# Performance work log

Measured on AMD Instinct MI355X. Metric: run time of the kernel, lower is better.

The kernel has to match this reference:

```python
import jax, jax.numpy as jnp
import numpy as np

KS = 3  # kernel_size


def _im2col(x):
    # x: (N, C, H, W) -> (N, H*W, C*KS*KS), matching torch unfold (channel-major,
    # kernel-position-minor) ordering with padding=1.
    N, C, H, W = x.shape
    xp = jnp.pad(x, ((0, 0), (0, 0), (1, 1), (1, 1)))
    patches = jnp.stack(
        [xp[:, :, i:i + H, j:j + W] for i in range(KS) for j in range(KS)],
        axis=2,
    )  # (N, C, 9, H, W)
    return patches.reshape(N, C * KS * KS, H * W).transpose(0, 2, 1)


def setup_inputs() -> dict:
    key = jax.random.key(0)
    k1, k2, k3, k4, k5 = jax.random.split(key, 5)
    N, C, H, W = 4, 64, 192, 192
    outC = 3
    return {
        "lr_features": jax.random.normal(k1, (N, C, H, W), dtype=jnp.float32),
        "W1": jax.random.normal(k2, (3, 256), dtype=jnp.float32) * 0.05,
        "b1": jax.random.normal(k3, (256,), dtype=jnp.float32) * 0.05,
        "W2": jax.random.normal(k4, (256, KS * KS * C * outC), dtype=jnp.float32) * 0.05,
        "b2": jax.random.normal(k5, (KS * KS * C * outC,), dtype=jnp.float32) * 0.05,
        "sr_scale": 4,
    }


def reference(lr_features, W1, b1, W2, b2, sr_scale):
    # Integer sr_scale: mask_mat is all-true and pos_mat_small is the s*s grid
    # of sub-pixel offsets [1/s, i/s, j/s] for i, j in [0, s).
    N, C, H, W = lr_features.shape
    s = int(np.ceil(sr_scale))
    inv = 1.0 / float(sr_scale)
    off = jnp.arange(s, dtype=jnp.float32) * inv
    pos = jnp.stack(jnp.meshgrid(off, off, indexing="ij"), axis=-1).reshape(s * s, 2)
    pos = jnp.concatenate(
        [jnp.full((s * s, 1), inv, dtype=jnp.float32), pos], axis=1
    )  # (s^2, 3)

    # Pos2Weight MLP -> per-subpixel dynamic conv weights (s^2, C*9, outC)
    hidden = jax.nn.relu(pos @ W1 + b1)
    local_weight = (hidden @ W2 + b2).reshape(s * s, KS * KS * C, -1)
    outC = local_weight.shape[-1]

    cols = _im2col(lr_features)  # (N, H*W, C*9)
    # batched small matmul: each sub-pixel position has its own filter
    out = jnp.einsum("npk,sko->nspo", cols, local_weight)  # (N, s^2, H*W, outC)
    out = out.reshape(N, s, s, H, W, outC)
    out = out.transpose(0, 5, 3, 1, 4, 2).reshape(N, outC, s * H, s * W)
    return out
```

## Files before the change

### kernel.cpp

```cpp
#include <hip/hip_runtime.h>


#define HH   192
#define WWD  192
#define SS   4
#define OC   3
#define PO   48
#define HID  256
#define W2LD 1728
#define BUFS 21120

typedef short  bf16x8 __attribute__((ext_vector_type(8)));
typedef float  f32x4  __attribute__((ext_vector_type(4)));

static __device__ __forceinline__ short f2bf(float f) {
    unsigned u = __float_as_uint(f);
    unsigned r = (u + 0x7fffu + ((u >> 16) & 1u)) >> 16;
    return (short)r;
}

static __device__ __forceinline__ void pin(bf16x8& v) {
    asm volatile("" : "+v"(v));
}

__global__ __launch_bounds__(256) void prep_kernel(
        const float* __restrict__ x,
        const float* __restrict__ W1, const float* __restrict__ b1,
        const float* __restrict__ W2, const float* __restrict__ b2,
        short* __restrict__ lwb, short* __restrict__ xt) {
    const int b = blockIdx.x;
    const int t = threadIdx.x;
    if (b < 112) {
        __shared__ float hlds[HID];
        const int p = b / 7;
        {
            const float pi = (float)(p >> 2) * 0.25f;
            const float pj = (float)(p & 3) * 0.25f;
            const float v = 0.25f * W1[t] + pi * W1[HID + t] + pj * W1[2 * HID + t]
                          + b1[t];
            hlds[t] = v > 0.f ? v : 0.f;
        }
        __syncthreads();
        const int col = (b % 7) * 256 + t;
        if (col < W2LD) {
            float a = 0.f;
#pragma unroll 32
            for (int hh = 0; hh < HID; ++hh)
                a += hlds[hh] * W2[hh * W2LD + col];
            const int o = col % 3, kc = col / 3;
            const int tap = kc % 9, c = kc / 9;
            lwb[(tap * PO + p * 3 + o) * 64 + c] = f2bf(a + b2[col]);
        }
    } else {
        __shared__ short tl[64][72];
        const int bb = b - 112;
        const int wt = bb % 3;
        const int h  = (bb / 3) % HH;
        const int n  = bb / (3 * HH);
        const int w0 = wt * 64;
#pragma unroll
        for (int i = 0; i < 4; ++i) {
            const int idx = i * 256 + t;
            const int c   = idx >> 4;
            const int j4  = idx & 15;
            const float4 v = *(const float4*)
                &x[(((size_t)(n * 64 + c)) * HH + h) * WWD + w0 + j4 * 4];
            tl[j4 * 4 + 0][c] = f2bf(v.x);
            tl[j4 * 4 + 1][c] = f2bf(v.y);
            tl[j4 * 4 + 2][c] = f2bf(v.z);
            tl[j4 * 4 + 3][c] = f2bf(v.w);
        }
        __syncthreads();
        const int w  = t >> 2;
        const int c0 = (t & 3) * 16;
        short* dst = &xt[(((size_t)n * HH + h) * WWD + w0 + w) * 64 + c0];
        *(bf16x8*)&dst[0] = *(const bf16x8*)&tl[w][c0];
        *(bf16x8*)&dst[8] = *(const bf16x8*)&tl[w][c0 + 8];
    }
}

__global__ __launch_bounds__(384) void meta_up_mfma(
        const short* __restrict__ xt, const short* __restrict__ lwb,
        float* __restrict__ out) {
    __shared__ __align__(16) short smem[2 * BUFS + 18720];
    float* obuf = (float*)&smem[2 * BUFS];

    const int xcd = blockIdx.x & 7;
    const int ii  = blockIdx.x >> 3;
    const int tid = threadIdx.x;
    const int lane = tid & 63;
    const int wv   = (tid >> 6) % 3;
    const int wgq  = (tid >> 6) / 3;
    const int quad = lane >> 4, l15 = lane & 15;

    bf16x8 Bf[18];
#pragma unroll
    for (int tap = 0; tap < 9; ++tap)
#pragma unroll
        for (int kc2 = 0; kc2 < 2; ++kc2)
            Bf[tap * 2 + kc2] = *(const bf16x8*)
                &lwb[(tap * PO + wv * 16 + l15) * 64 + kc2 * 32 + quad * 8];
#pragma unroll
    for (int i = 0; i < 18; ++i) pin(Bf[i]);

    int n_c, h0_c, w0_c;
    {
        const int tau = 96 * xcd + 3 * ii;
        n_c = tau / 192;
        const int rem = tau % 192;
        w0_c = (rem / 64) * 64;
        h0_c = (rem % 64) * 3;
    }

    const bf16x8 z = {0, 0, 0, 0, 0, 0, 0, 0};
    bf16x8 sv[7];

#pragma unroll
    for (int k = 0; k < 7; ++k) {
        const int item = k * 384 + tid;
        const int r  = item / 528;
        const int rm = item - r * 528;
        const int j  = rm >> 3, cb = rm & 7;
        const int gr = h0_c - 1 + r, gc = w0_c - 1 + j;
        const bool ok = (item < 2640) && ((unsigned)gr < (unsigned)HH) &&
                        ((unsigned)gc < (unsigned)WWD);
        sv[k] = ok ? *(const bf16x8*)
            &xt[((size_t)(n_c * HH + gr) * WWD + gc) * 64 + cb * 8] : z;
    }
#pragma unroll
    for (int k = 0; k < 7; ++k) {
        const int item = k * 384 + tid;
        if (item < 2640) {
            const int r  = item / 528;
            const int rm = item - r * 528;
            const int j  = rm >> 3, cb = rm & 7;
            *(bf16x8*)&smem[(r * 66 + j) * 64 + ((cb ^ (j & 7)) << 3)] = sv[k];
        }
    }
    __syncthreads();

    for (int t = 0; t < 3; ++t) {
        int n_n = n_c, h0_n = h0_c, w0_n = w0_c;
        if (t < 2) {
            const int tau = 96 * xcd + 3 * ii + t + 1;
            n_n = tau / 192;
            const int rem = tau % 192;
            w0_n = (rem / 64) * 64;
            h0_n = (rem % 64) * 3;
#pragma unroll
            for (int k = 0; k < 7; ++k) {
                const int item = k * 384 + tid;
                const int r  = item / 528;
                const int rm = item - r * 528;
                const int j  = rm >> 3, cb = rm & 7;
                const int gr = h0_n - 1 + r, gc = w0_n - 1 + j;
                const bool ok = (item < 2640) && ((unsigned)gr < (unsigned)HH) &&
                                ((unsigned)gc < (unsigned)WWD);
                sv[k] = ok ? *(const bf16x8*)
                    &xt[((size_t)(n_n * HH + gr) * WWD + gc) * 64 + cb * 8] : z;
            }
        }

        const short* __restrict__ xb = &smem[(t & 1) * BUFS];
        f32x4 acc[3][2];
#pragma unroll
        for (int ih = 0; ih < 3; ++ih)
#pragma unroll
            for (int mtl = 0; mtl < 2; ++mtl)
                acc[ih][mtl] = (f32x4){0.f, 0.f, 0.f, 0.f};

#pragma unroll
        for (int b = 0; b < 6; ++b) {
            const int dj = b >> 1, kc2 = b & 1;
#pragma unroll
            for (int mtl = 0; mtl < 2; ++mtl) {
                const int mt  = wgq * 2 + mtl;
                const int col = mt * 16 + l15 + dj;
                const int blk = (kc2 * 4 + quad) ^ (col & 7);
#pragma unroll
                for (int r = 0; r < 5; ++r) {
                    bf16x8 a = *(const bf16x8*)&xb[(r * 66 + col) * 64 + (blk << 3)];
#pragma unroll
                    for (int di = 0; di < 3; ++di) {
                        const int ih = r - di;
                        if (ih >= 0 && ih < 3)
                            acc[ih][mtl] = __builtin_amdgcn_mfma_f32_16x16x32_bf16(
                                a, Bf[(di * 3 + dj) * 2 + kc2], acc[ih][mtl], 0, 0, 0);
                    }
                }
            }
        }

        {
            const int po = wv * 16 + l15;
            const int o  = po % 3;
            const int p  = po / 3;
            const int si = p >> 2, sj = p & 3;
            const int osi = o * 4 + si;
#pragma unroll
            for (int ih = 0; ih < 3; ++ih)
#pragma unroll
                for (int mtl = 0; mtl < 2; ++mtl) {
                    const int mt = wgq * 2 + mtl;
#pragma unroll
                    for (int r4 = 0; r4 < 4; ++r4) {
                        const int wl = mt * 16 + quad * 4 + r4;
                        obuf[(ih * 12 + osi) * 260 + wl * 4 + sj] = acc[ih][mtl][r4];
                    }
                }
        }
        __syncthreads();

#pragma unroll
        for (int ih = 0; ih < 3; ++ih)
#pragma unroll
            for (int h2 = 0; h2 < 2; ++h2) {
                const int idx = h2 * 384 + tid;
                const int osi = idx >> 6;
                const int c4  = idx & 63;
                const int o = osi >> 2, si = osi & 3;
                const int hh = h0_c + ih;
                const size_t base =
                    ((size_t)(n_c * OC + o) * (SS * HH) + (size_t)(SS * hh + si))
                        * (SS * WWD) + (size_t)(4 * w0_c) + c4 * 4;
                *(float4*)&out[base] =
                    *(const float4*)&obuf[(ih * 12 + osi) * 260 + c4 * 4];
            }

        if (t < 2) {
#pragma unroll
            for (int k = 0; k < 7; ++k) {
                const int item = k * 384 + tid;
                if (item < 2640) {
                    const int r  = item / 528;
                    const int rm = item - r * 528;
                    const int j  = rm >> 3, cb = rm & 7;
                    *(bf16x8*)&smem[((t + 1) & 1) * BUFS +
                        (r * 66 + j) * 64 + ((cb ^ (j & 7)) << 3)] = sv[k];
                }
            }
            __syncthreads();
            n_c = n_n; h0_c = h0_n; w0_c = w0_n;
        }
    }
}

extern "C" void kernel_launch(void* const* d_in, const int* in_sizes, int n_in,
                              void* d_out, int out_size, void* d_ws, size_t ws_size,
                              hipStream_t stream) {
    const float* x  = (const float*)d_in[0];
    const float* W1 = (const float*)d_in[1];
    const float* b1 = (const float*)d_in[2];
    const float* W2 = (const float*)d_in[3];
    const float* b2 = (const float*)d_in[4];
    float* out = (float*)d_out;
    short* lwb = (short*)d_ws;
    short* xt  = (short*)d_ws + 32768;

    prep_kernel<<<112 + 4 * HH * 3, 256, 0, stream>>>(x, W1, b1, W2, b2, lwb, xt);
    meta_up_mfma<<<256, 384, 0, stream>>>(xt, lwb, out);
}
```

Measured before the change: 112.4 us.

## Fuse NCHW-to-NHWC bf16 transpose into main MFMA kernel's tile loads

Result: slower. 116.0 us (+3.1%).

```diff
diff --git a/kernel.cpp b/kernel.cpp
--- a/kernel.cpp
+++ b/kernel.cpp
@@ -9,6 +9,7 @@
 #define HID  256
 #define W2LD 1728
 #define BUFS 21120
+#define CST  (HH * WWD)
 
 typedef short  bf16x8 __attribute__((ext_vector_type(8)));
 typedef float  f32x4  __attribute__((ext_vector_type(4)));
@@ -23,64 +24,80 @@
     asm volatile("" : "+v"(v));
 }
 
-__global__ __launch_bounds__(256) void prep_kernel(
-        const float* __restrict__ x,
+__global__ __launch_bounds__(256) void lw_kernel(
         const float* __restrict__ W1, const float* __restrict__ b1,
         const float* __restrict__ W2, const float* __restrict__ b2,
-        short* __restrict__ lwb, short* __restrict__ xt) {
+        short* __restrict__ lwb) {
+    __shared__ float hlds[HID];
     const int b = blockIdx.x;
     const int t = threadIdx.x;
-    if (b < 112) {
-        __shared__ float hlds[HID];
-        const int p = b / 7;
-        {
-            const float pi = (float)(p >> 2) * 0.25f;
-            const float pj = (float)(p & 3) * 0.25f;
-            const float v = 0.25f * W1[t] + pi * W1[HID + t] + pj * W1[2 * HID + t]
-                          + b1[t];
-            hlds[t] = v > 0.f ? v : 0.f;
-        }
-        __syncthreads();
-        const int col = (b % 7) * 256 + t;
-        if (col < W2LD) {
-            float a = 0.f;
+    const int p = b / 7;
+    {
+        const float pi = (float)(p >> 2) * 0.25f;
+        const float pj = (float)(p & 3) * 0.25f;
+        const float v = 0.25f * W1[t] + pi * W1[HID + t] + pj * W1[2 * HID + t]
+                      + b1[t];
+        hlds[t] = v > 0.f ? v : 0.f;
+    }
+    __syncthreads();
+    const int col = (b % 7) * 256 + t;
+    if (col < W2LD) {
+        float a = 0.f;
 #pragma unroll 32
-            for (int hh = 0; hh < HID; ++hh)
-                a += hlds[hh] * W2[hh * W2LD + col];
-            const int o = col % 3, kc = col / 3;
-            const int tap = kc % 9, c = kc / 9;
-            lwb[(tap * PO + p * 3 + o) * 64 + c] = f2bf(a + b2[col]);
-        }
-    } else {
-        __shared__ short tl[64][72];
-        const int bb = b - 112;
-        const int wt = bb % 3;
-        const int h  = (bb / 3) % HH;
-        const int n  = bb / (3 * HH);
-        const int w0 = wt * 64;
-#pragma unroll
-        for (int i = 0; i < 4; ++i) {
-            const int idx = i * 256 + t;
-            const int c   = idx >> 4;
-            const int j4  = idx & 15;
-            const float4 v = *(const float4*)
-                &x[(((size_t)(n * 64 + c)) * HH + h) * WWD + w0 + j4 * 4];
-            tl[j4 * 4 + 0][c] = f2bf(v.x);
-            tl[j4 * 4 + 1][c] = f2bf(v.y);
-            tl[j4 * 4 + 2][c] = f2bf(v.z);
-            tl[j4 * 4 + 3][c] = f2bf(v.w);
-        }
-        __syncthreads();
-        const int w  = t >> 2;
-        const int c0 = (t & 3) * 16;
-        short* dst = &xt[(((size_t)n * HH + h) * WWD + w0 + w) * 64 + c0];
-        *(bf16x8*)&dst[0] = *(const bf16x8*)&tl[w][c0];
-        *(bf16x8*)&dst[8] = *(const bf16x8*)&tl[w][c0 + 8];
-    }
-}
-
-__global__ __launch_bounds__(384) void meta_up_mfma(
-        const short* __restrict__ xt, const short* __restrict__ lwb,
+        for (int hh = 0; hh < HID; ++hh)
+            a += hlds[hh] * W2[hh * W2LD + col];
+        const int o = col % 3, kc = col / 3;
+        const int tap = kc % 9, c = kc / 9;
+        lwb[(tap * PO + p * 3 + o) * 64 + c] = f2bf(a + b2[col]);
+    }
+}
+
+static __device__ __forceinline__ void stage_load(
+        const float* __restrict__ x, int n, int h0, int w0, int tid,
+        float fv[7][8]) {
+#pragma unroll
+    for (int k = 0; k < 7; ++k) {
+        const int item = k * 384 + tid;
+        const int r  = item / 528;
+        const int rm = item - r * 528;
+        const int cb = rm / 66;
+        const int j  = rm - cb * 66;
+        const int gr = h0 - 1 + r, gc = w0 - 1 + j;
+        const int grc = (unsigned)gr < (unsigned)HH ? gr : 0;
+        const int gcc = (unsigned)gc < (unsigned)WWD ? gc : 0;
+        const float* __restrict__ p = x +
+            ((size_t)(n * 64 + cb * 8) * HH + grc) * WWD + gcc;
+#pragma unroll
+        for (int cc = 0; cc < 8; ++cc)
+            fv[k][cc] = p[(size_t)cc * CST];
+    }
+}
+
+static __device__ __forceinline__ void stage_write(
+        short* __restrict__ buf, int h0, int w0, int tid,
+        const float fv[7][8]) {
+#pragma unroll
+    for (int k = 0; k < 7; ++k) {
+        const int item = k * 384 + tid;
+        if (item < 2640) {
+            const int r  = item / 528;
+            const int rm = item - r * 528;
+            const int cb = rm / 66;
+            const int j  = rm - cb * 66;
+            const int gr = h0 - 1 + r, gc = w0 - 1 + j;
+            const bool ok = ((unsigned)gr < (unsigned)HH) &&
+                            ((unsigned)gc < (unsigned)WWD);
+            bf16x8 pk;
+#pragma unroll
+            for (int cc = 0; cc < 8; ++cc)
+                pk[cc] = f2bf(ok ? fv[k][cc] : 0.f);
+            *(bf16x8*)&buf[(r * 66 + j) * 64 + ((cb ^ (j & 7)) << 3)] = pk;
+        }
+    }
+}
+
+__global__ __launch_bounds__(384, 1) void meta_up_mfma(
+        const float* __restrict__ x, const short* __restrict__ lwb,
         float* __restrict__ out) {
     __shared__ __align__(16) short smem[2 * BUFS + 18720];
     float* obuf = (float*)&smem[2 * BUFS];
@@ -112,31 +129,9 @@
         h0_c = (rem % 64) * 3;
     }
 
-    const bf16x8 z = {0, 0, 0, 0, 0, 0, 0, 0};
-    bf16x8 sv[7];
-
-#pragma unroll
-    for (int k = 0; k < 7; ++k) {
-        const int item = k * 384 + tid;
-        const int r  = item / 528;
-        const int rm = item - r * 528;
-        const int j  = rm >> 3, cb = rm & 7;
-        const int gr = h0_c - 1 + r, gc = w0_c - 1 + j;
-        const bool ok = (item < 2640) && ((unsigned)gr < (unsigned)HH) &&
-                        ((unsigned)gc < (unsigned)WWD);
-        sv[k] = ok ? *(const bf16x8*)
-            &xt[((size_t)(n_c * HH + gr) * WWD + gc) * 64 + cb * 8] : z;
-    }
-#pragma unroll
-    for (int k = 0; k < 7; ++k) {
-        const int item = k * 384 + tid;
-        if (item < 2640) {
-            const int r  = item / 528;
-            const int rm = item - r * 528;
-            const int j  = rm >> 3, cb = rm & 7;
-            *(bf16x8*)&smem[(r * 66 + j) * 64 + ((cb ^ (j & 7)) << 3)] = sv[k];
-        }
-    }
+    float fv[7][8];
+    stage_load(x, n_c, h0_c, w0_c, tid, fv);
+    stage_write(smem, h0_c, w0_c, tid, fv);
     __syncthreads();
 
     for (int t = 0; t < 3; ++t) {
@@ -147,18 +142,7 @@
             const int rem = tau % 192;
             w0_n = (rem / 64) * 64;
             h0_n = (rem % 64) * 3;
-#pragma unroll
-            for (int k = 0; k < 7; ++k) {
-                const int item = k * 384 + tid;
-                const int r  = item / 528;
-                const int rm = item - r * 528;
-                const int j  = rm >> 3, cb = rm & 7;
-                const int gr = h0_n - 1 + r, gc = w0_n - 1 + j;
-                const bool ok = (item < 2640) && ((unsigned)gr < (unsigned)HH) &&
-                                ((unsigned)gc < (unsigned)WWD);
-                sv[k] = ok ? *(const bf16x8*)
-                    &xt[((size_t)(n_n * HH + gr) * WWD + gc) * 64 + cb * 8] : z;
-            }
+            stage_load(x, n_n, h0_n, w0_n, tid, fv);
         }
 
         const short* __restrict__ xb = &smem[(t & 1) * BUFS];
@@ -228,17 +212,7 @@
             }
 
         if (t < 2) {
-#pragma unroll
-            for (int k = 0; k < 7; ++k) {
-                const int item = k * 384 + tid;
-                if (item < 2640) {
-                    const int r  = item / 528;
-                    const int rm = item - r * 528;
-                    const int j  = rm >> 3, cb = rm & 7;
-                    *(bf16x8*)&smem[((t + 1) & 1) * BUFS +
-                        (r * 66 + j) * 64 + ((cb ^ (j & 7)) << 3)] = sv[k];
-                }
-            }
+            stage_write(&smem[((t + 1) & 1) * BUFS], h0_n, w0_n, tid, fv);
             __syncthreads();
             n_c = n_n; h0_c = h0_n; w0_c = w0_n;
         }
@@ -255,8 +229,7 @@
     const float* b2 = (const float*)d_in[4];
     float* out = (float*)d_out;
     short* lwb = (short*)d_ws;
-    short* xt  = (short*)d_ws + 32768;
-
-    prep_kernel<<<112 + 4 * HH * 3, 256, 0, stream>>>(x, W1, b1, W2, b2, lwb, xt);
-    meta_up_mfma<<<256, 384, 0, stream>>>(xt, lwb, out);
-}
+
+    lw_kernel<<<112, 256, 0, stream>>>(W1, b1, W2, b2, lwb);
+    meta_up_mfma<<<256, 384, 0, stream>>>(x, lwb, out);
+}
```
